# Performance work log

Measured on AMD Instinct MI355X. Metric: run time of the kernel, lower is better.

Reference implementation:

```python
import jax, jax.numpy as jnp
import numpy as np

RS = [(16, 0, 0), (16, 1, 0), (16, 2, 0)]  # same list for Rs_in and Rs_out
BATCH = 262144


def _dim(Rs):
    return sum(mul * (2 * l + 1) for mul, l, _ in Rs)


def _build_mixing_and_norm():
    """Replicates rs.tensor_product(Rs_out, Rs_in, selection_rule lmax=0).

    Each path k connects one (mul_out index v, mul_in index u) pair within a
    matching irrep (l,p), with CG coefficient delta_{mm'} / sqrt(2l+1).
    norm_coef[i,j] = 1/sqrt(num_summed/mul_out) = 1/sqrt(sum mul_in) on the
    diagonal irrep blocks (eye(len(Rs_out)) * factors expanded to elements).
    """
    Rs_in, Rs_out = RS, RS
    dim_in, dim_out = _dim(Rs_in), _dim(Rs_out)
    in_off = np.cumsum([0] + [mul * (2 * l + 1) for mul, l, _ in Rs_in])
    out_off = np.cumsum([0] + [mul * (2 * l + 1) for mul, l, _ in Rs_out])
    K = sum(vo * ui for (vo, lo, po) in Rs_out for (ui, li, pi) in Rs_in
            if (lo, po) == (li, pi))
    mixing = np.zeros((K, dim_out, dim_in), np.float32)
    norm = np.zeros((dim_out, dim_in), np.float32)
    k = 0
    for n, (mul_out, l_out, p_out) in enumerate(Rs_out):
        num_summed = sum(mul_in * mul_out for mul_in, l_in, p_in in Rs_in
                         if (l_in, p_in) == (l_out, p_out))
        factor = 1.0 / np.sqrt(num_summed / mul_out)
        for m, (mul_in, l_in, p_in) in enumerate(Rs_in):
            if (l_in, p_in) != (l_out, p_out):
                continue
            d = 2 * l_out + 1
            cg = 1.0 / np.sqrt(d)
            for v in range(mul_out):
                for u in range(mul_in):
                    i0 = out_off[n] + v * d
                    j0 = in_off[m] + u * d
                    for t in range(d):
                        mixing[k, i0 + t, j0 + t] = cg
                    k += 1
            if n == m:  # eye(len(Rs_out)) in original norm_coef
                norm[out_off[n]:out_off[n + 1], in_off[m]:in_off[m + 1]] = factor
    return jnp.asarray(mixing), jnp.asarray(norm)


def setup_inputs() -> dict:
    key = jax.random.key(0)
    k_feat, k_w = jax.random.split(key)
    dim = _dim(RS)
    mixing, norm = _build_mixing_and_norm()
    features = jax.random.normal(k_feat, (BATCH, dim), dtype=jnp.float32)
    weight = jax.random.normal(k_w, (mixing.shape[0],), dtype=jnp.float32)
    return {"features": features, "weight": weight,
            "mixing_matrix": mixing, "norm_coef": norm}


def reference(features, weight, mixing_matrix, norm_coef):
    # torch.einsum('kij,k,zj,ij->zi', mixing, weight, features, norm)
    # Assemble the batch-independent weight once, then one dense GEMM.
    W = jnp.einsum('kij,k->ij', mixing_matrix, weight) * norm_coef  # [I, J]
    return jnp.einsum('zj,ij->zi', features, W)                    # [Z, I]
```

## Files before the change

### kernel.cpp

```cpp
#include <hip/hip_runtime.h>

#define DIM 144
#define ROWS 64
#define TILE_ELEMS (ROWS * DIM)
#define TILE_F4 (TILE_ELEMS / 4)
#define F4_PER_THREAD (TILE_F4 / 256)

__global__ __launch_bounds__(256) void build_C(
    const float* __restrict__ weight,
    const float* __restrict__ mixing,
    const float* __restrict__ norm,
    float* __restrict__ Cw)
{
    int idx = blockIdx.x * 256 + threadIdx.x;
    if (idx >= 9 * 256) return;
    int p  = idx >> 8;
    int vu = idx & 255;
    int v = vu >> 4, u = vu & 15;
    int l, t, off;
    if (p == 0)      { l = 0; t = 0;     off = 0;  }
    else if (p < 4)  { l = 1; t = p - 1; off = 16; }
    else             { l = 2; t = p - 4; off = 64; }
    int d  = 2 * l + 1;
    int k  = l * 256 + v * 16 + u;
    int i0 = off + v * d + t;
    int j0 = off + u * d + t;
    float m  = mixing[(size_t)k * (DIM * DIM) + i0 * DIM + j0];
    float nc = norm[i0 * DIM + j0];
    Cw[idx] = m * nc * weight[k];
}

__device__ __forceinline__ void unit_params(int p, int& d, int& t, int& off) {
    int l;
    if (p == 0)      { l = 0; t = 0;     off = 0;  }
    else if (p < 4)  { l = 1; t = p - 1; off = 16; }
    else             { l = 2; t = p - 4; off = 64; }
    d = 2 * l + 1;
}

__global__ __launch_bounds__(256) void tp_linear_kernel(
    const float4* __restrict__ feat4,
    const float* __restrict__ Cw,
    float4* __restrict__ out4,
    long long total4)
{
    __shared__ float buf[DIM * 64];
    const int tid = threadIdx.x;
    const long long base4 = (long long)blockIdx.x * TILE_F4;
    const bool full = (base4 + TILE_F4 <= total4);

    float4 v[F4_PER_THREAD];
    if (full) {
#pragma unroll
        for (int i = 0; i < F4_PER_THREAD; ++i)
            v[i] = feat4[base4 + i * 256 + tid];
    } else {
#pragma unroll
        for (int i = 0; i < F4_PER_THREAD; ++i) {
            long long g = base4 + i * 256 + tid;
            v[i] = (g < total4) ? feat4[g] : make_float4(0.f, 0.f, 0.f, 0.f);
        }
    }
#pragma unroll
    for (int i = 0; i < F4_PER_THREAD; ++i) {
        int e4  = i * 256 + tid;
        int row = e4 / 36;
        int c   = e4 - row * 36;
        float* p = &buf[(4 * c) * 64 + (row ^ c)];
        p[0]       = v[i].x;
        p[64]      = v[i].y;
        p[128]     = v[i].z;
        p[192]     = v[i].w;
    }
    __syncthreads();

    const int r = tid & 63;
    const int w = tid >> 6;
    for (int p = w; p < 9; p += 4) {
        int d, t, off;
        unit_params(p, d, t, off);
        const float* __restrict__ C = Cw + p * 256;

        float fin[16];
#pragma unroll
        for (int u = 0; u < 16; ++u) {
            int col = off + u * d + t;
            fin[u] = buf[col * 64 + (r ^ (col >> 2))];
        }
        float acc[16];
#pragma unroll
        for (int vv = 0; vv < 16; ++vv) {
            float a = 0.0f;
#pragma unroll
            for (int u = 0; u < 16; ++u)
                a += C[vv * 16 + u] * fin[u];
            acc[vv] = a;
        }
#pragma unroll
        for (int vv = 0; vv < 16; ++vv) {
            int col = off + vv * d + t;
            buf[col * 64 + (r ^ (col >> 2))] = acc[vv];
        }
    }
    __syncthreads();

#pragma unroll
    for (int i = 0; i < F4_PER_THREAD; ++i) {
        int e4  = i * 256 + tid;
        int row = e4 / 36;
        int c   = e4 - row * 36;
        const float* p = &buf[(4 * c) * 64 + (row ^ c)];
        float4 o = make_float4(p[0], p[64], p[128], p[192]);
        if (full) {
            out4[base4 + e4] = o;
        } else {
            long long g = base4 + e4;
            if (g < total4) out4[g] = o;
        }
    }
}

extern "C" void kernel_launch(void* const* d_in, const int* in_sizes, int n_in,
                              void* d_out, int out_size, void* d_ws, size_t ws_size,
                              hipStream_t stream)
{
    const float* feat   = (const float*)d_in[0];
    const float* weight = (const float*)d_in[1];
    const float* mixing = (const float*)d_in[2];
    const float* norm   = (const float*)d_in[3];
    float* out = (float*)d_out;
    float* Cw  = (float*)d_ws;

    long long total  = (long long)in_sizes[0];
    long long total4 = total / 4;
    int nrows = (int)(total / DIM);
    int tiles = (nrows + ROWS - 1) / ROWS;

    build_C<<<9, 256, 0, stream>>>(weight, mixing, norm, Cw);
    tp_linear_kernel<<<tiles, 256, 0, stream>>>(
        (const float4*)feat, Cw, (float4*)out, total4);
}
```

Measured before the change: 333.0 us.

## Make tp_linear kernel persistent with register double-buffered tile prefetch

Launches a fixed grid of 1024 persistent blocks that stride over the 64-row tiles. While the current tile is computed in shared memory, the next tile's features are prefetched into a second register buffer, so global load latency overlaps with compute. The cost is doubled register use for the tile buffers (launch bounds now request 4 blocks per CU) and an extra barrier per iteration. It may also reduce occupancy or cause register spills, and the kernel stays memory-bound.

```diff
diff --git a/kernel.cpp b/kernel.cpp
--- a/kernel.cpp
+++ b/kernel.cpp
@@ -5,6 +5,7 @@
 #define TILE_ELEMS (ROWS * DIM)
 #define TILE_F4 (TILE_ELEMS / 4)
 #define F4_PER_THREAD (TILE_F4 / 256)
+#define PERSIST_BLOCKS 1024
 
 __global__ __launch_bounds__(256) void build_C(
     const float* __restrict__ weight,
@@ -38,19 +39,11 @@
     d = 2 * l + 1;
 }
 
-__global__ __launch_bounds__(256) void tp_linear_kernel(
-    const float4* __restrict__ feat4,
-    const float* __restrict__ Cw,
-    float4* __restrict__ out4,
-    long long total4)
+__device__ __forceinline__ void load_tile(
+    const float4* __restrict__ feat4, long long base4, long long total4,
+    int tid, float4 v[F4_PER_THREAD])
 {
-    __shared__ float buf[DIM * 64];
-    const int tid = threadIdx.x;
-    const long long base4 = (long long)blockIdx.x * TILE_F4;
-    const bool full = (base4 + TILE_F4 <= total4);
-
-    float4 v[F4_PER_THREAD];
-    if (full) {
+    if (base4 + TILE_F4 <= total4) {
 #pragma unroll
         for (int i = 0; i < F4_PER_THREAD; ++i)
             v[i] = feat4[base4 + i * 256 + tid];
@@ -61,62 +54,95 @@
             v[i] = (g < total4) ? feat4[g] : make_float4(0.f, 0.f, 0.f, 0.f);
         }
     }
+}
+
+__global__ __launch_bounds__(256, 4) void tp_linear_kernel(
+    const float4* __restrict__ feat4,
+    const float* __restrict__ Cw,
+    float4* __restrict__ out4,
+    long long total4,
+    int tiles)
+{
+    __shared__ float buf[DIM * 64];
+    const int tid = threadIdx.x;
+    const int nb  = gridDim.x;
+    const int r   = tid & 63;
+    const int w   = tid >> 6;
+
+    int t = blockIdx.x;
+    if (t >= tiles) return;
+
+    float4 va[F4_PER_THREAD], vb[F4_PER_THREAD];
+    load_tile(feat4, (long long)t * TILE_F4, total4, tid, va);
+
+    for (; t < tiles; t += nb) {
 #pragma unroll
-    for (int i = 0; i < F4_PER_THREAD; ++i) {
-        int e4  = i * 256 + tid;
-        int row = e4 / 36;
-        int c   = e4 - row * 36;
-        float* p = &buf[(4 * c) * 64 + (row ^ c)];
-        p[0]       = v[i].x;
-        p[64]      = v[i].y;
-        p[128]     = v[i].z;
-        p[192]     = v[i].w;
-    }
-    __syncthreads();
+        for (int i = 0; i < F4_PER_THREAD; ++i) {
+            int e4  = i * 256 + tid;
+            int row = e4 / 36;
+            int c   = e4 - row * 36;
+            float* p = &buf[(4 * c) * 64 + (row ^ c)];
+            p[0]   = va[i].x;
+            p[64]  = va[i].y;
+            p[128] = va[i].z;
+            p[192] = va[i].w;
+        }
 
-    const int r = tid & 63;
-    const int w = tid >> 6;
-    for (int p = w; p < 9; p += 4) {
-        int d, t, off;
-        unit_params(p, d, t, off);
-        const float* __restrict__ C = Cw + p * 256;
+        int tn = t + nb;
+        if (tn < tiles)
+            load_tile(feat4, (long long)tn * TILE_F4, total4, tid, vb);
 
-        float fin[16];
+        __syncthreads();
+
+        for (int p = w; p < 9; p += 4) {
+            int d, tt, off;
+            unit_params(p, d, tt, off);
+            const float* __restrict__ C = Cw + p * 256;
+
+            float fin[16];
 #pragma unroll
-        for (int u = 0; u < 16; ++u) {
-            int col = off + u * d + t;
-            fin[u] = buf[col * 64 + (r ^ (col >> 2))];
+            for (int u = 0; u < 16; ++u) {
+                int col = off + u * d + tt;
+                fin[u] = buf[col * 64 + (r ^ (col >> 2))];
+            }
+            float acc[16];
+#pragma unroll
+            for (int vv = 0; vv < 16; ++vv) {
+                float a = 0.0f;
+#pragma unroll
+                for (int u = 0; u < 16; ++u)
+                    a += C[vv * 16 + u] * fin[u];
+                acc[vv] = a;
+            }
+#pragma unroll
+            for (int vv = 0; vv < 16; ++vv) {
+                int col = off + vv * d + tt;
+                buf[col * 64 + (r ^ (col >> 2))] = acc[vv];
+            }
         }
-        float acc[16];
+        __syncthreads();
+
+        long long base4 = (long long)t * TILE_F4;
+        bool full = (base4 + TILE_F4 <= total4);
 #pragma unroll
-        for (int vv = 0; vv < 16; ++vv) {
-            float a = 0.0f;
-#pragma unroll
-            for (int u = 0; u < 16; ++u)
-                a += C[vv * 16 + u] * fin[u];
-            acc[vv] = a;
+        for (int i = 0; i < F4_PER_THREAD; ++i) {
+            int e4  = i * 256 + tid;
+            int row = e4 / 36;
+            int c   = e4 - row * 36;
+            const float* p = &buf[(4 * c) * 64 + (row ^ c)];
+            float4 o = make_float4(p[0], p[64], p[128], p[192]);
+            if (full) {
+                out4[base4 + e4] = o;
+            } else {
+                long long g = base4 + e4;
+                if (g < total4) out4[g] = o;
+            }
         }
-#pragma unroll
-        for (int vv = 0; vv < 16; ++vv) {
-            int col = off + vv * d + t;
-            buf[col * 64 + (r ^ (col >> 2))] = acc[vv];
-        }
-    }
-    __syncthreads();
+
+        __syncthreads();
 
 #pragma unroll
-    for (int i = 0; i < F4_PER_THREAD; ++i) {
-        int e4  = i * 256 + tid;
-        int row = e4 / 36;
-        int c   = e4 - row * 36;
-        const float* p = &buf[(4 * c) * 64 + (row ^ c)];
-        float4 o = make_float4(p[0], p[64], p[128], p[192]);
-        if (full) {
-            out4[base4 + e4] = o;
-        } else {
-            long long g = base4 + e4;
-            if (g < total4) out4[g] = o;
-        }
+        for (int i = 0; i < F4_PER_THREAD; ++i) va[i] = vb[i];
     }
 }
 
@@ -135,8 +161,9 @@
     long long total4 = total / 4;
     int nrows = (int)(total / DIM);
     int tiles = (nrows + ROWS - 1) / ROWS;
+    int nb    = tiles < PERSIST_BLOCKS ? tiles : PERSIST_BLOCKS;
 
     build_C<<<9, 256, 0, stream>>>(weight, mixing, norm, Cw);
-    tp_linear_kernel<<<tiles, 256, 0, stream>>>(
-        (const float4*)feat, Cw, (float4*)out, total4);
+    tp_linear_kernel<<<nb, 256, 0, stream>>>(
+        (const float4*)feat, Cw, (float4*)out, total4, tiles);
 }
```

Result: slower. 345.1 us (+3.6%).
